# Kernel tuning notes

Measured on AMD Instinct MI355X. Metric: run time of the kernel, lower is better.

## Reference

```python
import jax, jax.numpy as jnp
import numpy as np

B = 131072
IN_FEAT = 128
OUT_FEAT = 128
RANK = 32


def setup_inputs() -> dict:
    key = jax.random.key(0)
    k1, k2, k3, k4, k5 = jax.random.split(key, 5)
    inp = jax.random.normal(k1, (B, IN_FEAT), dtype=jnp.float32)
    # per-sample generated weight flattened [B, r*r], as passed to set_parameters
    gen_weight = jax.random.normal(k2, (B, RANK * RANK), dtype=jnp.float32) * 0.05
    U = jax.random.normal(k3, (IN_FEAT, RANK), dtype=jnp.float32) * (1.0 / np.sqrt(IN_FEAT))
    V = jax.random.normal(k4, (RANK, OUT_FEAT), dtype=jnp.float32) * (1.0 / np.sqrt(RANK))
    bias = jax.random.normal(k5, (OUT_FEAT,), dtype=jnp.float32) * 0.01
    return {"inp": inp, "gen_weight": gen_weight, "U": U, "V": V, "bias": bias}


def reference(inp, gen_weight, U, V, bias):
    # U_matrix projection: [B, I] -> [B, r]
    h = inp @ U
    # per-sample generated weight: [B, r*r] -> [B, r, r]
    W = gen_weight.reshape(-1, RANK, RANK)
    # (h.unsqueeze(-1) * W).sum(-2) == batched GEMV: [B, r]
    h = jnp.einsum('bi,bio->bo', h, W)
    # V_matrix projection + bias: [B, r] -> [B, O]
    out = h @ V + bias
    return out
```

## Files before the change

### kernel.cpp

```cpp
#include <hip/hip_runtime.h>


constexpr int RANK  = 32;
constexpr int BLOCK = 256;
constexpr int WPB   = BLOCK / 64;
constexpr int GRID  = 1024;
constexpr int NWAVES = GRID * WPB;

typedef int i2_t __attribute__((ext_vector_type(2)));

__device__ __forceinline__ float bcast(float v, int srclane) {
    return __uint_as_float(__builtin_amdgcn_readlane(__float_as_uint(v), srclane));
}

__device__ __forceinline__ float red_xor8(float v) {
#if __has_builtin(__builtin_amdgcn_update_dpp)
    int m = __builtin_amdgcn_update_dpp(0, __float_as_int(v), 0x128, 0xf, 0xf, true);
    return v + __int_as_float(m);
#else
    return v + __shfl_xor(v, 8, 64);
#endif
}

__device__ __forceinline__ float red_xor16(float v) {
#if __has_builtin(__builtin_amdgcn_permlane16_swap)
    i2_t r = __builtin_amdgcn_permlane16_swap(__float_as_int(v), __float_as_int(v),
                                              false, false);
    return __int_as_float(r.x) + __int_as_float(r.y);
#else
    return v + __shfl_xor(v, 16, 64);
#endif
}

__device__ __forceinline__ float red_xor32(float v) {
#if __has_builtin(__builtin_amdgcn_permlane32_swap)
    i2_t r = __builtin_amdgcn_permlane32_swap(__float_as_int(v), __float_as_int(v),
                                              false, false);
    return __int_as_float(r.x) + __int_as_float(r.y);
#else
    return v + __shfl_xor(v, 32, 64);
#endif
}

__device__ __forceinline__ float red_g(float v) {
    return red_xor32(red_xor16(red_xor8(v)));
}

__global__ __launch_bounds__(BLOCK, 2)
void apg_linear_kernel(const float* __restrict__ inp,
                       const float* __restrict__ gw,
                       const float* __restrict__ U,
                       const float* __restrict__ V,
                       const float* __restrict__ bias,
                       float* __restrict__ out,
                       int nrows)
{
    __shared__ float4 u4s[1024];
    __shared__ float  hbuf[WPB][RANK];

    const int tid  = threadIdx.x;
    const int lane = tid & 63;
    const int wid  = tid >> 6;
    const int g    = lane >> 3;

    #pragma unroll
    for (int j = 0; j < 4; ++j)
        u4s[j * BLOCK + tid] = reinterpret_cast<const float4*>(U)[j * BLOCK + tid];
    __syncthreads();

    float2 v2[RANK];
    #pragma unroll
    for (int r = 0; r < RANK; ++r)
        v2[r] = reinterpret_cast<const float2*>(V + r * 128)[lane];
    const float2 b2 = reinterpret_cast<const float2*>(bias)[lane];

    float* hw = hbuf[wid];

    const int wave0 = blockIdx.x * WPB + wid;
    const int iters = (nrows + NWAVES - 1) / NWAVES;

    int row = wave0;
    float x0n = 0.f, x1n = 0.f;
    float4 w4n[4] = {};
    if (row < nrows) {
        x0n = inp[row * 128 + lane];
        x1n = inp[row * 128 + 64 + lane];
        const float4* wp = reinterpret_cast<const float4*>(gw) + row * 256;
        #pragma unroll
        for (int t = 0; t < 4; ++t) w4n[t] = wp[t * 64 + lane];
    }

    for (int it = 0; it < iters; ++it) {
        if (row >= nrows) break;
        const float x0 = x0n, x1 = x1n;
        float4 w4[4];
        #pragma unroll
        for (int t = 0; t < 4; ++t) w4[t] = w4n[t];

        const int nrow = row + NWAVES;
        if (it + 1 < iters && nrow < nrows) {
            x0n = inp[nrow * 128 + lane];
            x1n = inp[nrow * 128 + 64 + lane];
            const float4* wp = reinterpret_cast<const float4*>(gw) + nrow * 256;
            #pragma unroll
            for (int t = 0; t < 4; ++t) w4n[t] = wp[t * 64 + lane];
        }

        float h1a[4] = {0.f, 0.f, 0.f, 0.f};
        #pragma unroll
        for (int t = 0; t < 16; ++t) {
            const float xs = (t < 8) ? x0 : x1;
            const float xi = __shfl(xs, (t & 7) * 8 + g, 64);
            const float4 u = u4s[t * 64 + lane];
            h1a[0] = fmaf(xi, u.x, h1a[0]);
            h1a[1] = fmaf(xi, u.y, h1a[1]);
            h1a[2] = fmaf(xi, u.z, h1a[2]);
            h1a[3] = fmaf(xi, u.w, h1a[3]);
        }
        #pragma unroll
        for (int k = 0; k < 4; ++k) h1a[k] = red_g(h1a[k]);
        if (lane < 8)
            reinterpret_cast<float4*>(hw)[lane] =
                make_float4(h1a[0], h1a[1], h1a[2], h1a[3]);

        float h2a[4] = {0.f, 0.f, 0.f, 0.f};
        #pragma unroll
        for (int t = 0; t < 4; ++t) {
            const float hi = hw[t * 8 + g];
            h2a[0] = fmaf(hi, w4[t].x, h2a[0]);
            h2a[1] = fmaf(hi, w4[t].y, h2a[1]);
            h2a[2] = fmaf(hi, w4[t].z, h2a[2]);
            h2a[3] = fmaf(hi, w4[t].w, h2a[3]);
        }
        #pragma unroll
        for (int k = 0; k < 4; ++k) h2a[k] = red_g(h2a[k]);

        float o0 = b2.x, o1 = b2.y;
        #pragma unroll
        for (int r = 0; r < RANK; ++r) {
            const float h2r = bcast(h2a[r & 3], r >> 2);
            o0 = fmaf(h2r, v2[r].x, o0);
            o1 = fmaf(h2r, v2[r].y, o1);
        }
        reinterpret_cast<float2*>(out)[row * 64 + lane] = make_float2(o0, o1);

        row = nrow;
    }
}

extern "C" void kernel_launch(void* const* d_in, const int* in_sizes, int n_in,
                              void* d_out, int out_size, void* d_ws, size_t ws_size,
                              hipStream_t stream)
{
    const float* inp  = (const float*)d_in[0];
    const float* gw   = (const float*)d_in[1];
    const float* U    = (const float*)d_in[2];
    const float* V    = (const float*)d_in[3];
    const float* bias = (const float*)d_in[4];
    float* out = (float*)d_out;
    const int nrows = in_sizes[0] / 128;

    apg_linear_kernel<<<GRID, BLOCK, 0, stream>>>(inp, gw, U, V, bias, out, nrows);
}
```

Baseline: 129.9 us.

## Double-buffer row prefetch, pack V into fp16 dot2, raise occupancy bound

Restructures the per-wave loop to keep two rows in flight (A/B buffers) with prefetch two strides ahead, issued mid-computation to hide global memory latency. The V projection uses packed fp16 operands with v_dot2 (fdot2), halving V register storage and FMA count. Launch bounds raised to 4 blocks/CU to increase occupancy. Risks fp16 precision loss in V and h2, plus register pressure from the extra prefetch buffers.

```diff
diff --git a/kernel.cpp b/kernel.cpp
--- a/kernel.cpp
+++ b/kernel.cpp
@@ -7,11 +7,10 @@
 constexpr int GRID  = 1024;
 constexpr int NWAVES = GRID * WPB;
 
-typedef int i2_t __attribute__((ext_vector_type(2)));
-
-__device__ __forceinline__ float bcast(float v, int srclane) {
-    return __uint_as_float(__builtin_amdgcn_readlane(__float_as_uint(v), srclane));
-}
+typedef int    i2_t __attribute__((ext_vector_type(2)));
+typedef __fp16 h2_t __attribute__((ext_vector_type(2)));
+
+#define USE_DOT2 (__has_builtin(__builtin_amdgcn_fdot2) && __has_builtin(__builtin_amdgcn_cvt_pkrtz))
 
 __device__ __forceinline__ float red_xor8(float v) {
 #if __has_builtin(__builtin_amdgcn_update_dpp)
@@ -21,7 +20,6 @@
     return v + __shfl_xor(v, 8, 64);
 #endif
 }
-
 __device__ __forceinline__ float red_xor16(float v) {
 #if __has_builtin(__builtin_amdgcn_permlane16_swap)
     i2_t r = __builtin_amdgcn_permlane16_swap(__float_as_int(v), __float_as_int(v),
@@ -31,7 +29,6 @@
     return v + __shfl_xor(v, 16, 64);
 #endif
 }
-
 __device__ __forceinline__ float red_xor32(float v) {
 #if __has_builtin(__builtin_amdgcn_permlane32_swap)
     i2_t r = __builtin_amdgcn_permlane32_swap(__float_as_int(v), __float_as_int(v),
@@ -41,12 +38,26 @@
     return v + __shfl_xor(v, 32, 64);
 #endif
 }
-
 __device__ __forceinline__ float red_g(float v) {
     return red_xor32(red_xor16(red_xor8(v)));
 }
 
-__global__ __launch_bounds__(BLOCK, 2)
+__device__ __forceinline__ h2_t rl_h2(int packed, int srclane) {
+    int i = __builtin_amdgcn_readlane(packed, srclane);
+    h2_t r; __builtin_memcpy(&r, &i, 4);
+    return r;
+}
+__device__ __forceinline__ int pack_h2(float a, float b) {
+#if USE_DOT2
+    auto p = __builtin_amdgcn_cvt_pkrtz(a, b);
+    int i; __builtin_memcpy(&i, &p, 4);
+    return i;
+#else
+    return 0;
+#endif
+}
+
+__global__ __launch_bounds__(BLOCK, 4)
 void apg_linear_kernel(const float* __restrict__ inp,
                        const float* __restrict__ gw,
                        const float* __restrict__ U,
@@ -68,10 +79,21 @@
         u4s[j * BLOCK + tid] = reinterpret_cast<const float4*>(U)[j * BLOCK + tid];
     __syncthreads();
 
+#if USE_DOT2
+    h2_t v2a[16], v2b[16];
+    #pragma unroll
+    for (int s = 0; s < 16; ++s) {
+        const float2 r0 = reinterpret_cast<const float2*>(V + (2*s)     * 128)[lane];
+        const float2 r1 = reinterpret_cast<const float2*>(V + (2*s + 1) * 128)[lane];
+        v2a[s] = h2_t{(__fp16)r0.x, (__fp16)r1.x};
+        v2b[s] = h2_t{(__fp16)r0.y, (__fp16)r1.y};
+    }
+#else
     float2 v2[RANK];
     #pragma unroll
     for (int r = 0; r < RANK; ++r)
         v2[r] = reinterpret_cast<const float2*>(V + r * 128)[lane];
+#endif
     const float2 b2 = reinterpret_cast<const float2*>(bias)[lane];
 
     float* hw = hbuf[wid];
@@ -79,33 +101,27 @@
     const int wave0 = blockIdx.x * WPB + wid;
     const int iters = (nrows + NWAVES - 1) / NWAVES;
 
-    int row = wave0;
-    float x0n = 0.f, x1n = 0.f;
-    float4 w4n[4] = {};
-    if (row < nrows) {
-        x0n = inp[row * 128 + lane];
-        x1n = inp[row * 128 + 64 + lane];
-        const float4* wp = reinterpret_cast<const float4*>(gw) + row * 256;
-        #pragma unroll
-        for (int t = 0; t < 4; ++t) w4n[t] = wp[t * 64 + lane];
-    }
-
-    for (int it = 0; it < iters; ++it) {
-        if (row >= nrows) break;
-        const float x0 = x0n, x1 = x1n;
-        float4 w4[4];
-        #pragma unroll
-        for (int t = 0; t < 4; ++t) w4[t] = w4n[t];
-
-        const int nrow = row + NWAVES;
-        if (it + 1 < iters && nrow < nrows) {
-            x0n = inp[nrow * 128 + lane];
-            x1n = inp[nrow * 128 + 64 + lane];
-            const float4* wp = reinterpret_cast<const float4*>(gw) + nrow * 256;
-            #pragma unroll
-            for (int t = 0; t < 4; ++t) w4n[t] = wp[t * 64 + lane];
-        }
-
+    float  x0A = 0.f, x1A = 0.f, x0B = 0.f, x1B = 0.f;
+    float4 wA[4] = {}, wB[4] = {};
+
+    const int rA0 = wave0;
+    const int rB0 = wave0 + NWAVES;
+    if (rA0 < nrows) {
+        x0A = inp[rA0 * 128 + lane];
+        x1A = inp[rA0 * 128 + 64 + lane];
+        const float4* wp = reinterpret_cast<const float4*>(gw) + rA0 * 256;
+        #pragma unroll
+        for (int t = 0; t < 4; ++t) wA[t] = wp[t * 64 + lane];
+    }
+    if (rB0 < nrows) {
+        x0B = inp[rB0 * 128 + lane];
+        x1B = inp[rB0 * 128 + 64 + lane];
+        const float4* wp = reinterpret_cast<const float4*>(gw) + rB0 * 256;
+        #pragma unroll
+        for (int t = 0; t < 4; ++t) wB[t] = wp[t * 64 + lane];
+    }
+
+    auto process = [&](int row, float& x0, float& x1, float4 (&w4)[4], int prow) {
         float h1a[4] = {0.f, 0.f, 0.f, 0.f};
         #pragma unroll
         for (int t = 0; t < 16; ++t) {
@@ -132,19 +148,50 @@
             h2a[2] = fmaf(hi, w4[t].z, h2a[2]);
             h2a[3] = fmaf(hi, w4[t].w, h2a[3]);
         }
+
+        if (prow < nrows) {
+            x0 = inp[prow * 128 + lane];
+            x1 = inp[prow * 128 + 64 + lane];
+            const float4* wp = reinterpret_cast<const float4*>(gw) + prow * 256;
+            #pragma unroll
+            for (int t = 0; t < 4; ++t) w4[t] = wp[t * 64 + lane];
+        }
+
         #pragma unroll
         for (int k = 0; k < 4; ++k) h2a[k] = red_g(h2a[k]);
 
         float o0 = b2.x, o1 = b2.y;
+#if USE_DOT2
+        const int h2p0 = pack_h2(h2a[0], h2a[1]);
+        const int h2p1 = pack_h2(h2a[2], h2a[3]);
+        #pragma unroll
+        for (int c = 0; c < 8; ++c) {
+            const h2_t p0 = rl_h2(h2p0, c);
+            const h2_t p1 = rl_h2(h2p1, c);
+            o0 = __builtin_amdgcn_fdot2(p0, v2a[2*c],     o0, false);
+            o1 = __builtin_amdgcn_fdot2(p0, v2b[2*c],     o1, false);
+            o0 = __builtin_amdgcn_fdot2(p1, v2a[2*c + 1], o0, false);
+            o1 = __builtin_amdgcn_fdot2(p1, v2b[2*c + 1], o1, false);
+        }
+#else
         #pragma unroll
         for (int r = 0; r < RANK; ++r) {
-            const float h2r = bcast(h2a[r & 3], r >> 2);
+            const float h2r = __uint_as_float(
+                __builtin_amdgcn_readlane(__float_as_uint(h2a[r & 3]), r >> 2));
             o0 = fmaf(h2r, v2[r].x, o0);
             o1 = fmaf(h2r, v2[r].y, o1);
         }
+#endif
         reinterpret_cast<float2*>(out)[row * 64 + lane] = make_float2(o0, o1);
-
-        row = nrow;
+    };
+
+    for (int it = 0; it < iters; it += 2) {
+        const int rowA = wave0 + it * NWAVES;
+        const int rowB = rowA + NWAVES;
+        if (rowA >= nrows) break;
+        process(rowA, x0A, x1A, wA, rowA + 2 * NWAVES);
+        if (rowB >= nrows) break;
+        process(rowB, x0B, x1B, wB, rowB + 2 * NWAVES);
     }
 }
 
```

Result: slower. 141.1 us (+8.6%).

## Use packed fp16 dot2 for U and V projections with swizzled LDS layout

Applied to the files above, without the earlier changes.

Converts input rows, U and V to packed half-precision pairs and computes the U and V projections with v_dot2 instructions, halving FMA count and LDS traffic for U. U is stored in LDS as packed pairs with an XOR swizzle to avoid bank conflicts, and each lane now loads its input elements as a float2. The kernel is memory-bound on reading gen_weight, so compute savings may matter little, and the fp16 rounding of inputs and weights reduces accuracy.

```diff
diff --git a/kernel.cpp b/kernel.cpp
--- a/kernel.cpp
+++ b/kernel.cpp
@@ -7,11 +7,8 @@
 constexpr int GRID  = 1024;
 constexpr int NWAVES = GRID * WPB;
 
-typedef int i2_t __attribute__((ext_vector_type(2)));
-
-__device__ __forceinline__ float bcast(float v, int srclane) {
-    return __uint_as_float(__builtin_amdgcn_readlane(__float_as_uint(v), srclane));
-}
+typedef int    i2_t __attribute__((ext_vector_type(2)));
+typedef __fp16 h2_t __attribute__((ext_vector_type(2)));
 
 __device__ __forceinline__ float red_xor8(float v) {
 #if __has_builtin(__builtin_amdgcn_update_dpp)
@@ -21,7 +18,6 @@
     return v + __shfl_xor(v, 8, 64);
 #endif
 }
-
 __device__ __forceinline__ float red_xor16(float v) {
 #if __has_builtin(__builtin_amdgcn_permlane16_swap)
     i2_t r = __builtin_amdgcn_permlane16_swap(__float_as_int(v), __float_as_int(v),
@@ -31,7 +27,6 @@
     return v + __shfl_xor(v, 16, 64);
 #endif
 }
-
 __device__ __forceinline__ float red_xor32(float v) {
 #if __has_builtin(__builtin_amdgcn_permlane32_swap)
     i2_t r = __builtin_amdgcn_permlane32_swap(__float_as_int(v), __float_as_int(v),
@@ -41,9 +36,21 @@
     return v + __shfl_xor(v, 32, 64);
 #endif
 }
-
 __device__ __forceinline__ float red_g(float v) {
     return red_xor32(red_xor16(red_xor8(v)));
+}
+
+__device__ __forceinline__ int pack_h2(float a, float b) {
+    auto p = __builtin_amdgcn_cvt_pkrtz(a, b);
+    int i; __builtin_memcpy(&i, &p, 4);
+    return i;
+}
+__device__ __forceinline__ h2_t as_h2(int i) {
+    h2_t r; __builtin_memcpy(&r, &i, 4);
+    return r;
+}
+__device__ __forceinline__ h2_t rl_h2(int packed, int srclane) {
+    return as_h2(__builtin_amdgcn_readlane(packed, srclane));
 }
 
 __global__ __launch_bounds__(BLOCK, 2)
@@ -55,23 +62,32 @@
                        float* __restrict__ out,
                        int nrows)
 {
-    __shared__ float4 u4s[1024];
-    __shared__ float  hbuf[WPB][RANK];
+    __shared__ int   u2s[2048];
+    __shared__ float hbuf[WPB][RANK];
 
     const int tid  = threadIdx.x;
     const int lane = tid & 63;
     const int wid  = tid >> 6;
     const int g    = lane >> 3;
+    const int c    = lane & 7;
 
-    #pragma unroll
-    for (int j = 0; j < 4; ++j)
-        u4s[j * BLOCK + tid] = reinterpret_cast<const float4*>(U)[j * BLOCK + tid];
+    for (int e = tid; e < 2048; e += BLOCK) {
+        const int i2 = e >> 5, j = e & 31;
+        const float a = U[(2 * i2) * 32 + j];
+        const float b = U[(2 * i2 + 1) * 32 + j];
+        const int blk = (j >> 2) ^ (i2 & 7);
+        u2s[i2 * 32 + blk * 4 + (j & 3)] = pack_h2(a, b);
+    }
     __syncthreads();
 
-    float2 v2[RANK];
+    h2_t v2a[16], v2b[16];
     #pragma unroll
-    for (int r = 0; r < RANK; ++r)
-        v2[r] = reinterpret_cast<const float2*>(V + r * 128)[lane];
+    for (int s = 0; s < 16; ++s) {
+        const float2 r0 = reinterpret_cast<const float2*>(V + (2*s)     * 128)[lane];
+        const float2 r1 = reinterpret_cast<const float2*>(V + (2*s + 1) * 128)[lane];
+        v2a[s] = h2_t{(__fp16)r0.x, (__fp16)r1.x};
+        v2b[s] = h2_t{(__fp16)r0.y, (__fp16)r1.y};
+    }
     const float2 b2 = reinterpret_cast<const float2*>(bias)[lane];
 
     float* hw = hbuf[wid];
@@ -80,11 +96,11 @@
     const int iters = (nrows + NWAVES - 1) / NWAVES;
 
     int row = wave0;
-    float x0n = 0.f, x1n = 0.f;
+    int    xpkn = 0;
     float4 w4n[4] = {};
     if (row < nrows) {
-        x0n = inp[row * 128 + lane];
-        x1n = inp[row * 128 + 64 + lane];
+        const float2 xv = reinterpret_cast<const float2*>(inp + row * 128)[lane];
+        xpkn = pack_h2(xv.x, xv.y);
         const float4* wp = reinterpret_cast<const float4*>(gw) + row * 256;
         #pragma unroll
         for (int t = 0; t < 4; ++t) w4n[t] = wp[t * 64 + lane];
@@ -92,15 +108,15 @@
 
     for (int it = 0; it < iters; ++it) {
         if (row >= nrows) break;
-        const float x0 = x0n, x1 = x1n;
+        const int xpk = xpkn;
         float4 w4[4];
         #pragma unroll
         for (int t = 0; t < 4; ++t) w4[t] = w4n[t];
 
         const int nrow = row + NWAVES;
         if (it + 1 < iters && nrow < nrows) {
-            x0n = inp[nrow * 128 + lane];
-            x1n = inp[nrow * 128 + 64 + lane];
+            const float2 xv = reinterpret_cast<const float2*>(inp + nrow * 128)[lane];
+            xpkn = pack_h2(xv.x, xv.y);
             const float4* wp = reinterpret_cast<const float4*>(gw) + nrow * 256;
             #pragma unroll
             for (int t = 0; t < 4; ++t) w4n[t] = wp[t * 64 + lane];
@@ -108,14 +124,14 @@
 
         float h1a[4] = {0.f, 0.f, 0.f, 0.f};
         #pragma unroll
-        for (int t = 0; t < 16; ++t) {
-            const float xs = (t < 8) ? x0 : x1;
-            const float xi = __shfl(xs, (t & 7) * 8 + g, 64);
-            const float4 u = u4s[t * 64 + lane];
-            h1a[0] = fmaf(xi, u.x, h1a[0]);
-            h1a[1] = fmaf(xi, u.y, h1a[1]);
-            h1a[2] = fmaf(xi, u.z, h1a[2]);
-            h1a[3] = fmaf(xi, u.w, h1a[3]);
+        for (int t = 0; t < 8; ++t) {
+            const h2_t xp = as_h2(__shfl(xpk, t * 8 + g, 64));
+            const int4 uq = *reinterpret_cast<const int4*>(
+                &u2s[(t * 8 + g) * 32 + (c ^ g) * 4]);
+            h1a[0] = __builtin_amdgcn_fdot2(xp, as_h2(uq.x), h1a[0], false);
+            h1a[1] = __builtin_amdgcn_fdot2(xp, as_h2(uq.y), h1a[1], false);
+            h1a[2] = __builtin_amdgcn_fdot2(xp, as_h2(uq.z), h1a[2], false);
+            h1a[3] = __builtin_amdgcn_fdot2(xp, as_h2(uq.w), h1a[3], false);
         }
         #pragma unroll
         for (int k = 0; k < 4; ++k) h1a[k] = red_g(h1a[k]);
@@ -136,11 +152,16 @@
         for (int k = 0; k < 4; ++k) h2a[k] = red_g(h2a[k]);
 
         float o0 = b2.x, o1 = b2.y;
+        const int h2p0 = pack_h2(h2a[0], h2a[1]);
+        const int h2p1 = pack_h2(h2a[2], h2a[3]);
         #pragma unroll
-        for (int r = 0; r < RANK; ++r) {
-            const float h2r = bcast(h2a[r & 3], r >> 2);
-            o0 = fmaf(h2r, v2[r].x, o0);
-            o1 = fmaf(h2r, v2[r].y, o1);
+        for (int cc = 0; cc < 8; ++cc) {
+            const h2_t p0 = rl_h2(h2p0, cc);
+            const h2_t p1 = rl_h2(h2p1, cc);
+            o0 = __builtin_amdgcn_fdot2(p0, v2a[2*cc],     o0, false);
+            o1 = __builtin_amdgcn_fdot2(p0, v2b[2*cc],     o1, false);
+            o0 = __builtin_amdgcn_fdot2(p1, v2a[2*cc + 1], o0, false);
+            o1 = __builtin_amdgcn_fdot2(p1, v2b[2*cc + 1], o1, false);
         }
         reinterpret_cast<float2*>(out)[row * 64 + lane] = make_float2(o0, o1);
 
```

Measured after the change: 146.3 us. 12.6% more time.
